# Performance work log

Measured on AMD Instinct MI355X. Metric: run time of the kernel, lower is better.

The kernel has to match this reference:

```python
import jax, jax.numpy as jnp
import numpy as np

T, B, X, Y = 24, 16, 64, 64
S, M, C = 16, 8, 8
F = S + M + C   # GRU input_size = 32
H = 32          # hidden_size


def setup_inputs() -> dict:
    key = jax.random.key(0)
    ks = jax.random.split(key, 8)
    inv = 1.0 / np.sqrt(H)
    return {
        "spatial": jax.random.normal(ks[0], (T, B, X, Y, S), dtype=jnp.float32),
        "meteorology": jax.random.normal(ks[1], (T, B, X, Y, M), dtype=jnp.float32),
        "context": jax.random.normal(ks[2], (T, B, X, Y, C), dtype=jnp.float32),
        # GRU parameters (torch layout: [3H, F] and [3H, H], gate order r,z,n)
        "W_ih": jax.random.uniform(ks[3], (3 * H, F), jnp.float32, -inv, inv),
        "W_hh": jax.random.uniform(ks[4], (3 * H, H), jnp.float32, -inv, inv),
        "b_ih": jax.random.uniform(ks[5], (3 * H,), jnp.float32, -inv, inv),
        "b_hh": jax.random.uniform(ks[6], (3 * H,), jnp.float32, -inv, inv),
        # output projection (hidden -> spatial_size)
        "W": jax.random.normal(ks[7], (H, S), dtype=jnp.float32),
    }


def reference(spatial, meteorology, context, W_ih, W_hh, b_ih, b_hh, W):
    # cat features: (T, B, X, Y, F); merge all pixels + batch into one GRU batch
    x = jnp.concatenate((spatial, meteorology, context), axis=4)
    N = B * X * Y
    x = x.reshape(T, N, F)

    # precompute input projections for all timesteps: (T, N, 3H)
    gx_all = jnp.einsum('tnf,gf->tng', x, W_ih) + b_ih

    def step(h, gx):
        gh = h @ W_hh.T + b_hh                      # (N, 3H)
        r = jax.nn.sigmoid(gx[:, :H] + gh[:, :H])
        z = jax.nn.sigmoid(gx[:, H:2 * H] + gh[:, H:2 * H])
        n = jnp.tanh(gx[:, 2 * H:] + r * gh[:, 2 * H:])
        h = (1.0 - z) * n + z * h
        return h, None

    h0 = jnp.zeros((N, H), dtype=x.dtype)
    h_final, _ = jax.lax.scan(step, h0, gx_all)     # (N, H)

    out = h_final @ W                               # (N, S)
    return out.reshape(B, X, Y, S)
```

## Files before the change

### kernel.cpp

```cpp
#include <hip/hip_runtime.h>


#define TSTEPS 24
#define NPIX 65536
#define NWAVES 4096

typedef __attribute__((ext_vector_type(8))) short bf16x8;
typedef __attribute__((ext_vector_type(4))) float f32x4;

#define MFMA16(a, b, c) __builtin_amdgcn_mfma_f32_16x16x32_bf16((a), (b), (c), 0, 0, 0)

__device__ __forceinline__ unsigned short f2bf(float f) {
  unsigned u = __builtin_bit_cast(unsigned, f);
  u += 0x7fffu + ((u >> 16) & 1u);
  return (unsigned short)(u >> 16);
}

__device__ __forceinline__ float sigmoid_(float x) {
  return __builtin_amdgcn_rcpf(1.f + __expf(-x));
}
__device__ __forceinline__ float tanh_(float x) {
  return 1.f - 2.f * __builtin_amdgcn_rcpf(__expf(2.f * x) + 1.f);
}

__device__ __forceinline__ bf16x8 relayout_h(const f32x4 h0, const f32x4 h1,
                                             int q, int col) {
  bf16x8 r;
  const int rbase = (q & 1) * 8;
  const bool lowtile = (q < 2);
#pragma unroll
  for (int j = 0; j < 8; ++j) {
    int rr = rbase + j;
    int src = ((rr >> 2) << 4) | col;
    float v0 = __shfl(h0[j & 3], src, 64);
    float v1 = __shfl(h1[j & 3], src, 64);
    r[j] = f2bf(lowtile ? v0 : v1);
  }
  return r;
}

__global__ __launch_bounds__(256, 4)
void gru_fused(const float* __restrict__ spatial, const float* __restrict__ met,
               const float* __restrict__ ctx,
               const float* __restrict__ W_ih, const float* __restrict__ W_hh,
               const float* __restrict__ b_ih, const float* __restrict__ b_hh,
               const float* __restrict__ Wout, float* __restrict__ out) {
  __shared__ __align__(16) unsigned short sW[2 * 96 * 32];
  __shared__ __align__(16) float sCB[64];
  __shared__ __align__(16) float sBIN[32];
  __shared__ __align__(16) float sBHN[32];

  const int tid = threadIdx.x;
  for (int i = tid; i < 96 * 32; i += 256) {
    sW[i] = f2bf(W_ih[i]);
    sW[96 * 32 + i] = f2bf(W_hh[i]);
  }
  if (tid < 64) sCB[tid] = b_ih[tid] + b_hh[tid];
  else if (tid < 96) sBIN[tid - 64] = b_ih[tid];
  else if (tid < 128) sBHN[tid - 96] = b_hh[tid - 32];
  __syncthreads();

  const int wave = blockIdx.x * 4 + (tid >> 6);
  const int lane = tid & 63;
  const int col = lane & 15;
  const int q = lane >> 4;
  const long p = (long)wave * 16 + col;

  const float* xptr;
  long xstride;
  if (q < 2)       { xptr = spatial + p * 16 + q * 8; xstride = (long)NPIX * 16; }
  else if (q == 2) { xptr = met + p * 8;              xstride = (long)NPIX * 8;  }
  else             { xptr = ctx + p * 8;              xstride = (long)NPIX * 8;  }

  f32x4 h0 = {0.f, 0.f, 0.f, 0.f};
  f32x4 h1 = {0.f, 0.f, 0.f, 0.f};
  const f32x4 zero = {0.f, 0.f, 0.f, 0.f};

  f32x4 xa = *(const f32x4*)xptr;
  f32x4 xb = *(const f32x4*)(xptr + 4);
  xptr += xstride;

#pragma unroll 1
  for (int t = 0; t < TSTEPS; ++t) {
    bf16x8 bx;
#pragma unroll
    for (int j = 0; j < 4; ++j) { bx[j] = f2bf(xa[j]); bx[4 + j] = f2bf(xb[j]); }

    if (t < TSTEPS - 1) {
      xa = *(const f32x4*)xptr;
      xb = *(const f32x4*)(xptr + 4);
      xptr += xstride;
    }

    bf16x8 bh = relayout_h(h0, h1, q, col);

    f32x4 G[6], Hv[6];
#pragma unroll
    for (int i = 0; i < 4; ++i) {
      bf16x8 a = *(const bf16x8*)&sW[(i * 16 + col) * 32 + q * 8];
      G[i] = MFMA16(a, bx, *(const f32x4*)&sCB[i * 16 + q * 4]);
    }
    {
      bf16x8 a4 = *(const bf16x8*)&sW[(4 * 16 + col) * 32 + q * 8];
      G[4] = MFMA16(a4, bx, *(const f32x4*)&sBIN[q * 4]);
      bf16x8 a5 = *(const bf16x8*)&sW[(5 * 16 + col) * 32 + q * 8];
      G[5] = MFMA16(a5, bx, *(const f32x4*)&sBIN[16 + q * 4]);
    }
#pragma unroll
    for (int i = 0; i < 4; ++i) {
      bf16x8 a = *(const bf16x8*)&sW[96 * 32 + (i * 16 + col) * 32 + q * 8];
      Hv[i] = MFMA16(a, bh, zero);
    }
    {
      bf16x8 a4 = *(const bf16x8*)&sW[96 * 32 + (4 * 16 + col) * 32 + q * 8];
      Hv[4] = MFMA16(a4, bh, *(const f32x4*)&sBHN[q * 4]);
      bf16x8 a5 = *(const bf16x8*)&sW[96 * 32 + (5 * 16 + col) * 32 + q * 8];
      Hv[5] = MFMA16(a5, bh, *(const f32x4*)&sBHN[16 + q * 4]);
    }

#pragma unroll
    for (int r = 0; r < 4; ++r) {
      float rv0 = sigmoid_(G[0][r] + Hv[0][r]);
      float rv1 = sigmoid_(G[1][r] + Hv[1][r]);
      float zv0 = sigmoid_(G[2][r] + Hv[2][r]);
      float zv1 = sigmoid_(G[3][r] + Hv[3][r]);
      float nv0 = tanh_(G[4][r] + rv0 * Hv[4][r]);
      float nv1 = tanh_(G[5][r] + rv1 * Hv[5][r]);
      h0[r] = nv0 + zv0 * (h0[r] - nv0);
      h1[r] = nv1 + zv1 * (h1[r] - nv1);
    }
  }

  bf16x8 bhf = relayout_h(h0, h1, q, col);
  bf16x8 aw;
#pragma unroll
  for (int j = 0; j < 8; ++j) aw[j] = f2bf(Wout[(q * 8 + j) * 16 + col]);
  f32x4 o = MFMA16(aw, bhf, zero);
  *(f32x4*)&out[p * 16 + q * 4] = o;
}

extern "C" void kernel_launch(void* const* d_in, const int* in_sizes, int n_in,
                              void* d_out, int out_size, void* d_ws, size_t ws_size,
                              hipStream_t stream) {
  const float* spatial = (const float*)d_in[0];
  const float* met     = (const float*)d_in[1];
  const float* ctx     = (const float*)d_in[2];
  const float* W_ih    = (const float*)d_in[3];
  const float* W_hh    = (const float*)d_in[4];
  const float* b_ih    = (const float*)d_in[5];
  const float* b_hh    = (const float*)d_in[6];
  const float* Wout    = (const float*)d_in[7];
  float* out = (float*)d_out;

  gru_fused<<<dim3(NWAVES / 4), dim3(256), 0, stream>>>(
      spatial, met, ctx, W_ih, W_hh, b_ih, b_hh, Wout, out);
}
```

Baseline: 252.7 us.

## Keep W_hh in registers, chain MFMA accumulators, pack h before shuffles

```diff
diff --git a/kernel.cpp b/kernel.cpp
--- a/kernel.cpp
+++ b/kernel.cpp
@@ -3,10 +3,11 @@
 
 #define TSTEPS 24
 #define NPIX 65536
-#define NWAVES 4096
+#define PADW 40
 
 typedef __attribute__((ext_vector_type(8))) short bf16x8;
 typedef __attribute__((ext_vector_type(4))) float f32x4;
+typedef __attribute__((ext_vector_type(4))) unsigned int u32x4;
 
 #define MFMA16(a, b, c) __builtin_amdgcn_mfma_f32_16x16x32_bf16((a), (b), (c), 0, 0, 0)
 
@@ -16,6 +17,19 @@
   return (unsigned short)(u >> 16);
 }
 
+__device__ __forceinline__ unsigned pk2(float a, float b) {
+  unsigned ua = __builtin_bit_cast(unsigned, a);
+  unsigned ub = __builtin_bit_cast(unsigned, b);
+  ua += 0x7fffu + ((ua >> 16) & 1u);
+  ub += 0x7fffu + ((ub >> 16) & 1u);
+  return __builtin_amdgcn_perm(ub, ua, 0x07060302u);
+}
+
+__device__ __forceinline__ bf16x8 pack8(f32x4 a, f32x4 b) {
+  u32x4 r = { pk2(a[0], a[1]), pk2(a[2], a[3]), pk2(b[0], b[1]), pk2(b[2], b[3]) };
+  return __builtin_bit_cast(bf16x8, r);
+}
+
 __device__ __forceinline__ float sigmoid_(float x) {
   return __builtin_amdgcn_rcpf(1.f + __expf(-x));
 }
@@ -23,20 +37,22 @@
   return 1.f - 2.f * __builtin_amdgcn_rcpf(__expf(2.f * x) + 1.f);
 }
 
-__device__ __forceinline__ bf16x8 relayout_h(const f32x4 h0, const f32x4 h1,
-                                             int q, int col) {
-  bf16x8 r;
-  const int rbase = (q & 1) * 8;
-  const bool lowtile = (q < 2);
-#pragma unroll
-  for (int j = 0; j < 8; ++j) {
-    int rr = rbase + j;
-    int src = ((rr >> 2) << 4) | col;
-    float v0 = __shfl(h0[j & 3], src, 64);
-    float v1 = __shfl(h1[j & 3], src, 64);
-    r[j] = f2bf(lowtile ? v0 : v1);
-  }
-  return r;
+__device__ __forceinline__ bf16x8 relayout_h(const f32x4 h0, const f32x4 h1, int lane) {
+  unsigned p00 = pk2(h0[0], h0[1]), p01 = pk2(h0[2], h0[3]);
+  unsigned p10 = pk2(h1[0], h1[1]), p11 = pk2(h1[2], h1[3]);
+  const int lo = (lane & 15) | ((lane & 16) << 1);
+  const int hi = lo + 16;
+  unsigned a0 = (unsigned)__shfl((int)p00, lo, 64);
+  unsigned a1 = (unsigned)__shfl((int)p01, lo, 64);
+  unsigned a2 = (unsigned)__shfl((int)p00, hi, 64);
+  unsigned a3 = (unsigned)__shfl((int)p01, hi, 64);
+  unsigned b0 = (unsigned)__shfl((int)p10, lo, 64);
+  unsigned b1 = (unsigned)__shfl((int)p11, lo, 64);
+  unsigned b2 = (unsigned)__shfl((int)p10, hi, 64);
+  unsigned b3 = (unsigned)__shfl((int)p11, hi, 64);
+  const bool t1 = (lane & 32) != 0;
+  u32x4 d = { t1 ? b0 : a0, t1 ? b1 : a1, t1 ? b2 : a2, t1 ? b3 : a3 };
+  return __builtin_bit_cast(bf16x8, d);
 }
 
 __global__ __launch_bounds__(256, 4)
@@ -45,26 +61,35 @@
                const float* __restrict__ W_ih, const float* __restrict__ W_hh,
                const float* __restrict__ b_ih, const float* __restrict__ b_hh,
                const float* __restrict__ Wout, float* __restrict__ out) {
-  __shared__ __align__(16) unsigned short sW[2 * 96 * 32];
-  __shared__ __align__(16) float sCB[64];
-  __shared__ __align__(16) float sBIN[32];
-  __shared__ __align__(16) float sBHN[32];
+  __shared__ __align__(16) unsigned short sWih[96 * PADW];
 
   const int tid = threadIdx.x;
   for (int i = tid; i < 96 * 32; i += 256) {
-    sW[i] = f2bf(W_ih[i]);
-    sW[96 * 32 + i] = f2bf(W_hh[i]);
+    int r = i >> 5, c = i & 31;
+    sWih[r * PADW + c] = f2bf(W_ih[i]);
   }
-  if (tid < 64) sCB[tid] = b_ih[tid] + b_hh[tid];
-  else if (tid < 96) sBIN[tid - 64] = b_ih[tid];
-  else if (tid < 128) sBHN[tid - 96] = b_hh[tid - 32];
   __syncthreads();
 
-  const int wave = blockIdx.x * 4 + (tid >> 6);
   const int lane = tid & 63;
   const int col = lane & 15;
   const int q = lane >> 4;
+  const int wave = blockIdx.x * 4 + (tid >> 6);
   const long p = (long)wave * 16 + col;
+
+  bf16x8 whh[6];
+#pragma unroll
+  for (int i = 0; i < 6; ++i) {
+    const float* wp = W_hh + (i * 16 + col) * 32 + q * 8;
+    whh[i] = pack8(*(const f32x4*)wp, *(const f32x4*)(wp + 4));
+  }
+  f32x4 cS[4];
+#pragma unroll
+  for (int i = 0; i < 4; ++i)
+    cS[i] = *(const f32x4*)&b_ih[i * 16 + q * 4] + *(const f32x4*)&b_hh[i * 16 + q * 4];
+  const f32x4 cG4 = *(const f32x4*)&b_ih[64 + q * 4];
+  const f32x4 cG5 = *(const f32x4*)&b_ih[80 + q * 4];
+  const f32x4 cH4 = *(const f32x4*)&b_hh[64 + q * 4];
+  const f32x4 cH5 = *(const f32x4*)&b_hh[80 + q * 4];
 
   const float* xptr;
   long xstride;
@@ -72,69 +97,66 @@
   else if (q == 2) { xptr = met + p * 8;              xstride = (long)NPIX * 8;  }
   else             { xptr = ctx + p * 8;              xstride = (long)NPIX * 8;  }
 
+  bf16x8 bx = pack8(*(const f32x4*)xptr, *(const f32x4*)(xptr + 4));
+  xptr += xstride;
+
   f32x4 h0 = {0.f, 0.f, 0.f, 0.f};
   f32x4 h1 = {0.f, 0.f, 0.f, 0.f};
-  const f32x4 zero = {0.f, 0.f, 0.f, 0.f};
-
-  f32x4 xa = *(const f32x4*)xptr;
-  f32x4 xb = *(const f32x4*)(xptr + 4);
-  xptr += xstride;
 
 #pragma unroll 1
   for (int t = 0; t < TSTEPS; ++t) {
-    bf16x8 bx;
-#pragma unroll
-    for (int j = 0; j < 4; ++j) { bx[j] = f2bf(xa[j]); bx[4 + j] = f2bf(xb[j]); }
-
+    f32x4 xna, xnb;
     if (t < TSTEPS - 1) {
-      xa = *(const f32x4*)xptr;
-      xb = *(const f32x4*)(xptr + 4);
+      xna = *(const f32x4*)xptr;
+      xnb = *(const f32x4*)(xptr + 4);
       xptr += xstride;
     }
 
-    bf16x8 bh = relayout_h(h0, h1, q, col);
+    bf16x8 bh = relayout_h(h0, h1, lane);
 
-    f32x4 G[6], Hv[6];
-#pragma unroll
-    for (int i = 0; i < 4; ++i) {
-      bf16x8 a = *(const bf16x8*)&sW[(i * 16 + col) * 32 + q * 8];
-      G[i] = MFMA16(a, bx, *(const f32x4*)&sCB[i * 16 + q * 4]);
-    }
-    {
-      bf16x8 a4 = *(const bf16x8*)&sW[(4 * 16 + col) * 32 + q * 8];
-      G[4] = MFMA16(a4, bx, *(const f32x4*)&sBIN[q * 4]);
-      bf16x8 a5 = *(const bf16x8*)&sW[(5 * 16 + col) * 32 + q * 8];
-      G[5] = MFMA16(a5, bx, *(const f32x4*)&sBIN[16 + q * 4]);
-    }
-#pragma unroll
-    for (int i = 0; i < 4; ++i) {
-      bf16x8 a = *(const bf16x8*)&sW[96 * 32 + (i * 16 + col) * 32 + q * 8];
-      Hv[i] = MFMA16(a, bh, zero);
-    }
-    {
-      bf16x8 a4 = *(const bf16x8*)&sW[96 * 32 + (4 * 16 + col) * 32 + q * 8];
-      Hv[4] = MFMA16(a4, bh, *(const f32x4*)&sBHN[q * 4]);
-      bf16x8 a5 = *(const bf16x8*)&sW[96 * 32 + (5 * 16 + col) * 32 + q * 8];
-      Hv[5] = MFMA16(a5, bh, *(const f32x4*)&sBHN[16 + q * 4]);
-    }
+    const int wb = col * PADW + q * 8;
+    bf16x8 a0 = *(const bf16x8*)&sWih[wb];
+    bf16x8 a1 = *(const bf16x8*)&sWih[wb + 16 * PADW];
+    bf16x8 a2 = *(const bf16x8*)&sWih[wb + 32 * PADW];
+    bf16x8 a3 = *(const bf16x8*)&sWih[wb + 48 * PADW];
+    bf16x8 a4 = *(const bf16x8*)&sWih[wb + 64 * PADW];
+    bf16x8 a5 = *(const bf16x8*)&sWih[wb + 80 * PADW];
+
+    f32x4 g0 = MFMA16(a0, bx, cS[0]);
+    f32x4 g1 = MFMA16(a1, bx, cS[1]);
+    f32x4 g2 = MFMA16(a2, bx, cS[2]);
+    f32x4 g3 = MFMA16(a3, bx, cS[3]);
+    f32x4 G4 = MFMA16(a4, bx, cG4);
+    f32x4 G5 = MFMA16(a5, bx, cG5);
+    f32x4 S0 = MFMA16(whh[0], bh, g0);
+    f32x4 S1 = MFMA16(whh[1], bh, g1);
+    f32x4 S2 = MFMA16(whh[2], bh, g2);
+    f32x4 S3 = MFMA16(whh[3], bh, g3);
+    f32x4 H4 = MFMA16(whh[4], bh, cH4);
+    f32x4 H5 = MFMA16(whh[5], bh, cH5);
 
 #pragma unroll
     for (int r = 0; r < 4; ++r) {
-      float rv0 = sigmoid_(G[0][r] + Hv[0][r]);
-      float rv1 = sigmoid_(G[1][r] + Hv[1][r]);
-      float zv0 = sigmoid_(G[2][r] + Hv[2][r]);
-      float zv1 = sigmoid_(G[3][r] + Hv[3][r]);
-      float nv0 = tanh_(G[4][r] + rv0 * Hv[4][r]);
-      float nv1 = tanh_(G[5][r] + rv1 * Hv[5][r]);
+      float rv0 = sigmoid_(S0[r]);
+      float rv1 = sigmoid_(S1[r]);
+      float zv0 = sigmoid_(S2[r]);
+      float zv1 = sigmoid_(S3[r]);
+      float nv0 = tanh_(G4[r] + rv0 * H4[r]);
+      float nv1 = tanh_(G5[r] + rv1 * H5[r]);
       h0[r] = nv0 + zv0 * (h0[r] - nv0);
       h1[r] = nv1 + zv1 * (h1[r] - nv1);
     }
+
+    if (t < TSTEPS - 1) bx = pack8(xna, xnb);
   }
 
-  bf16x8 bhf = relayout_h(h0, h1, q, col);
-  bf16x8 aw;
+  bf16x8 bhf = relayout_h(h0, h1, lane);
+  float w[8];
 #pragma unroll
-  for (int j = 0; j < 8; ++j) aw[j] = f2bf(Wout[(q * 8 + j) * 16 + col]);
+  for (int j = 0; j < 8; ++j) w[j] = Wout[(q * 8 + j) * 16 + col];
+  u32x4 awp = { pk2(w[0], w[1]), pk2(w[2], w[3]), pk2(w[4], w[5]), pk2(w[6], w[7]) };
+  bf16x8 aw = __builtin_bit_cast(bf16x8, awp);
+  const f32x4 zero = {0.f, 0.f, 0.f, 0.f};
   f32x4 o = MFMA16(aw, bhf, zero);
   *(f32x4*)&out[p * 16 + q * 4] = o;
 }
@@ -152,6 +174,6 @@
   const float* Wout    = (const float*)d_in[7];
   float* out = (float*)d_out;
 
-  gru_fused<<<dim3(NWAVES / 4), dim3(256), 0, stream>>>(
+  gru_fused<<<dim3(NPIX / 16 / 4), dim3(256), 0, stream>>>(
       spatial, met, ctx, W_ih, W_hh, b_ih, b_hh, Wout, out);
 }
```

Measured after the change: 283.3 us. 1.12x slower.
